# Kernel optimization log

Hardware: AMD Instinct MI355X
Metric: run time of the kernel (lower is better)

The kernel has to match this reference:

```python
import jax, jax.numpy as jnp
import numpy as np

B, S, H, NH, HD = 4, 4096, 1024, 16, 64

def setup_inputs() -> dict:
    key = jax.random.key(0)
    ks = jax.random.split(key, 5)
    scale = 1.0 / np.sqrt(H)
    return {
        "hidden_states": jax.random.normal(ks[0], (B, S, H), dtype=jnp.float32),
        "Wq": jax.random.normal(ks[1], (H, H), dtype=jnp.float32) * scale,
        "Wk": jax.random.normal(ks[2], (H, H), dtype=jnp.float32) * scale,
        "Wv": jax.random.normal(ks[3], (H, H), dtype=jnp.float32) * scale,
        "Wo": jax.random.normal(ks[4], (H, H), dtype=jnp.float32) * scale,
    }

def reference(hidden_states, Wq, Wk, Wv, Wo):
    b, s, h = hidden_states.shape
    # torch nn.Linear: y = x @ W.T
    q = (hidden_states @ Wq.T).reshape(b, s, NH, HD)
    k = (hidden_states @ Wk.T).reshape(b, s, NH, HD)
    v = (hidden_states @ Wv.T).reshape(b, s, NH, HD)
    # feature map: ELU (as in source, no +1)
    q = jax.nn.elu(q)
    k = jax.nn.elu(k)
    # per-head kv state: sum over sequence of outer products k_s v_s^T -> [b,h,d,e]
    kv = jnp.einsum('bshd,bshe->bhde', k, v)
    out = jnp.einsum('bqhd,bhde->bqhe', q, kv)  # [b,s,h,e]
    out = out.reshape(b, s, h)
    return out @ Wo.T  # dropout p=0.0 is identity
```

## Files before the change

kernel.cpp:

```cpp
#include <hip/hip_runtime.h>
#include <cstdint>
#include <cstddef>

#define B_  4
#define S_  4096
#define H_  1024
#define NH_ 16
#define M_  (B_*S_)

typedef __bf16 bf16x8 __attribute__((ext_vector_type(8)));
typedef float  f32x4  __attribute__((ext_vector_type(4)));

__device__ __forceinline__ unsigned short f2b(float f) {
  union { float f; unsigned u; } v; v.f = f;
  unsigned r = v.u + 0x7FFFu + ((v.u >> 16) & 1u);
  return (unsigned short)(r >> 16);
}
__device__ __forceinline__ float b2f(unsigned short u) {
  union { unsigned u; float f; } v; v.u = ((unsigned)u) << 16;
  return v.f;
}

#define GLD16(g, l) __builtin_amdgcn_global_load_lds( \
    (const __attribute__((address_space(1))) void*)(g), \
    (__attribute__((address_space(3))) void*)(l), 16, 0, 0)

#define VM0()  asm volatile("s_waitcnt vmcnt(0)" ::: "memory")
#define VM2()  asm volatile("s_waitcnt vmcnt(2)" ::: "memory")
#define VM4()  asm volatile("s_waitcnt vmcnt(4)" ::: "memory")
#define BAR()  do { asm volatile("" ::: "memory"); __builtin_amdgcn_s_barrier(); \
                    asm volatile("" ::: "memory"); } while (0)

__global__ void cast_f32_bf16(const float* __restrict__ src,
                              unsigned short* __restrict__ dst, int n4) {
  int i = blockIdx.x * blockDim.x + threadIdx.x;
  if (i >= n4) return;
  float4 f = reinterpret_cast<const float4*>(src)[i];
  ushort4 o;
  o.x = f2b(f.x); o.y = f2b(f.y); o.z = f2b(f.z); o.w = f2b(f.w);
  reinterpret_cast<ushort4*>(dst)[i] = o;
}

__global__ void cast_w4(const float* __restrict__ w0, const float* __restrict__ w1,
                        const float* __restrict__ w2, const float* __restrict__ w3,
                        unsigned short* __restrict__ dst) {
  int i = blockIdx.x * blockDim.x + threadIdx.x;
  int w = i >> 18, j = i & 0x3FFFF;
  const float* src = (w == 0) ? w0 : (w == 1) ? w1 : (w == 2) ? w2 : w3;
  float4 f = reinterpret_cast<const float4*>(src)[j];
  ushort4 o;
  o.x = f2b(f.x); o.y = f2b(f.y); o.z = f2b(f.z); o.w = f2b(f.w);
  reinterpret_cast<ushort4*>(dst)[i] = o;
}

template<int MODE>
__global__ __launch_bounds__(512, 2) void gemm256(
    const unsigned short* __restrict__ A_,
    const unsigned short* __restrict__ Bt_,
    void* __restrict__ out) {
  __shared__ __align__(16) unsigned short LDS[2][2][16384];

  const int NTN = (MODE == 0) ? 12 : 4;
  const int nx  = gridDim.x >> 3;
  const int b2  = (blockIdx.x & 7) * nx + (blockIdx.x >> 3);
  const int tileM = (b2 / NTN) << 8;
  const int tileN = (b2 % NTN) << 8;

  const unsigned short* Bt_e =
      (MODE == 1) ? (Bt_ + ((size_t)(tileM >> 12) << 20)) : Bt_;

  const int tid  = threadIdx.x;
  const int lane = tid & 63, wv = tid >> 6;
  const int wmi  = wv >> 2;
  const int wni  = wv & 3;
  const int fr   = lane & 15, fq = lane >> 4;

  const int sr0 = tid >> 3,          sc0 = (tid & 7) ^ (sr0 & 7);
  const int sr1 = (tid + 512) >> 3,  sc1 = (tid & 7) ^ (sr1 & 7);

#define STG(NB, ARR, HM, SRC, RB, TT) do {                                      \
    GLD16((SRC) + (size_t)((RB) + (HM)*128 + sr0) * 1024 + (TT)*64 + sc0*8,     \
          &LDS[NB][ARR][(HM)*8192 + wv*512]);                                   \
    GLD16((SRC) + (size_t)((RB) + (HM)*128 + sr1) * 1024 + (TT)*64 + sc1*8,     \
          &LDS[NB][ARR][(HM)*8192 + 4096 + wv*512]);                            \
  } while (0)

#define LOADA(CB, MQ) do {                                                      \
    _Pragma("unroll")                                                           \
    for (int m = 0; m < 4; m++) {                                               \
      int r = (MQ)*128 + wmi*64 + m*16 + fr;                                    \
      af[m][0] = *(const bf16x8*)&LDS[CB][0][r*64 + ((fq    ) ^ (r&7))*8];      \
      af[m][1] = *(const bf16x8*)&LDS[CB][0][r*64 + ((4 + fq) ^ (r&7))*8];      \
    }                                                                           \
  } while (0)

#define LOADB(CB, NQ) do {                                                      \
    _Pragma("unroll")                                                           \
    for (int n = 0; n < 2; n++) {                                               \
      int r = (NQ)*128 + wni*32 + n*16 + fr;                                    \
      bv[n][0] = *(const bf16x8*)&LDS[CB][1][r*64 + ((fq    ) ^ (r&7))*8];      \
      bv[n][1] = *(const bf16x8*)&LDS[CB][1][r*64 + ((4 + fq) ^ (r&7))*8];      \
    }                                                                           \
  } while (0)

#define MM(MQ, NQ) do {                                                         \
    __builtin_amdgcn_s_setprio(1);                                              \
    _Pragma("unroll")                                                           \
    for (int m = 0; m < 4; m++)                                                 \
      _Pragma("unroll")                                                         \
      for (int n = 0; n < 2; n++) {                                             \
        acc[MQ][NQ][m][n] = __builtin_amdgcn_mfma_f32_16x16x32_bf16(            \
            af[m][0], bv[n][0], acc[MQ][NQ][m][n], 0, 0, 0);                    \
        acc[MQ][NQ][m][n] = __builtin_amdgcn_mfma_f32_16x16x32_bf16(            \
            af[m][1], bv[n][1], acc[MQ][NQ][m][n], 0, 0, 0);                    \
      }                                                                         \
    __builtin_amdgcn_s_setprio(0);                                              \
  } while (0)

  f32x4 zero = {0.f, 0.f, 0.f, 0.f};
  f32x4 acc[2][2][4][2];
#pragma unroll
  for (int a = 0; a < 2; a++)
#pragma unroll
    for (int b = 0; b < 2; b++)
#pragma unroll
      for (int m = 0; m < 4; m++)
#pragma unroll
        for (int n = 0; n < 2; n++) acc[a][b][m][n] = zero;

  bf16x8 af[4][2], bv[2][2];

  STG(0, 0, 0, A_,   tileM, 0);
  STG(0, 0, 1, A_,   tileM, 0);
  STG(0, 1, 0, Bt_e, tileN, 0);
  STG(0, 1, 1, Bt_e, tileN, 0);
  VM0();
  BAR();

  int cb = 0;
  for (int t = 0; t < 15; ++t) {
    const int nb = cb ^ 1;
    LOADA(cb, 0); LOADB(cb, 0);
    STG(nb, 0, 0, A_,   tileM, t + 1);
    BAR(); MM(0, 0); VM4(); BAR();
    LOADB(cb, 1);
    STG(nb, 1, 0, Bt_e, tileN, t + 1);
    BAR(); MM(0, 1); VM4(); BAR();
    LOADA(cb, 1);
    STG(nb, 1, 1, Bt_e, tileN, t + 1);
    BAR(); MM(1, 1); BAR();
    LOADB(cb, 0);
    STG(nb, 0, 1, A_,   tileM, t + 1);
    BAR(); MM(1, 0); VM4(); BAR();
    cb = nb;
  }
  LOADA(cb, 0); LOADB(cb, 0);
  BAR(); MM(0, 0); VM2(); BAR();
  LOADB(cb, 1);
  BAR(); MM(0, 1); VM0(); BAR();
  LOADA(cb, 1);
  BAR(); MM(1, 1); BAR();
  LOADB(cb, 0);
  BAR(); MM(1, 0);

  if (MODE == 0) {
    unsigned short* Ep = &LDS[0][0][0];
    const int reg = tileN >> 10;
    const bool doELU = (reg < 2);
    BAR();
#pragma unroll
    for (int mq = 0; mq < 2; mq++)
#pragma unroll
      for (int nq = 0; nq < 2; nq++)
#pragma unroll
        for (int m = 0; m < 4; m++)
#pragma unroll
          for (int n = 0; n < 2; n++)
#pragma unroll
            for (int r = 0; r < 4; r++) {
              int row = mq * 128 + wmi * 64 + m * 16 + fq * 4 + r;
              int col = nq * 128 + wni * 32 + n * 16 + fr;
              float v = acc[mq][nq][m][n][r];
              if (doELU) v = v > 0.f ? v : (expf(v) - 1.f);
              Ep[row * 256 + (col ^ ((row & 7) << 3))] = f2b(v);
            }
    BAR();
    unsigned short* outp = (unsigned short*)out + (size_t)reg * M_ * H_;
    const int lcbase = tileN & 1023;
#pragma unroll
    for (int it = 0; it < 16; it++) {
      int g = it * 512 + tid;
      int row = g >> 5, col = (g & 31) * 8;
      bf16x8 val = *(const bf16x8*)&Ep[row * 256 + (col ^ ((row & 7) << 3))];
      *(bf16x8*)&outp[(size_t)(tileM + row) * H_ + lcbase + col] = val;
    }
  } else {
    float* Ef = (float*)&LDS[0][0][0];
#pragma unroll
    for (int mq = 0; mq < 2; mq++) {
      BAR();
#pragma unroll
      for (int nq = 0; nq < 2; nq++)
#pragma unroll
        for (int m = 0; m < 4; m++)
#pragma unroll
          for (int n = 0; n < 2; n++)
#pragma unroll
            for (int r = 0; r < 4; r++) {
              int row = wmi * 64 + m * 16 + fq * 4 + r;
              int col = nq * 128 + wni * 32 + n * 16 + fr;
              Ef[row * 256 + (col ^ ((row & 7) << 2))] = acc[mq][nq][m][n][r];
            }
      BAR();
#pragma unroll
      for (int it = 0; it < 16; it++) {
        int g = it * 512 + tid;
        int row = g >> 6, c = (g & 63) * 4;
        f32x4 val = *(const f32x4*)&Ef[row * 256 + (c ^ ((row & 7) << 2))];
        *(f32x4*)&((float*)out)[(size_t)(tileM + mq * 128 + row) * H_ + tileN + c] = val;
      }
    }
  }
#undef MM
#undef LOADB
#undef LOADA
#undef STG
}

__global__ __launch_bounds__(256) void kv_partial(
    const unsigned short* __restrict__ Kb,
    const unsigned short* __restrict__ Vb,
    float* __restrict__ kvp) {
  __shared__ __align__(16) unsigned short kt[32 * 64];
  __shared__ __align__(16) unsigned short vt[32 * 64];
  const int bh = blockIdx.x >> 3;
  const int ch = blockIdx.x & 7;
  const int b  = bh >> 4, h = bh & 15;
  const int t  = threadIdx.x;
  const int rr = t >> 3;
  const int cc = (t & 7) * 8;
  const int d0 = (t >> 4) * 4;
  const int e0 = (t & 15) * 4;

  float acc[4][4] = {};
  for (int s0 = ch * 512; s0 < ch * 512 + 512; s0 += 32) {
    size_t g = (size_t)(b * S_ + s0 + rr) * H_ + h * 64 + cc;
    *reinterpret_cast<uint4*>(&kt[rr * 64 + cc]) = *reinterpret_cast<const uint4*>(Kb + g);
    *reinterpret_cast<uint4*>(&vt[rr * 64 + cc]) = *reinterpret_cast<const uint4*>(Vb + g);
    __syncthreads();
#pragma unroll 4
    for (int ss = 0; ss < 32; ss++) {
      ushort4 k4 = *reinterpret_cast<const ushort4*>(&kt[ss * 64 + d0]);
      ushort4 v4 = *reinterpret_cast<const ushort4*>(&vt[ss * 64 + e0]);
      float kf[4] = {b2f(k4.x), b2f(k4.y), b2f(k4.z), b2f(k4.w)};
      float vf[4] = {b2f(v4.x), b2f(v4.y), b2f(v4.z), b2f(v4.w)};
#pragma unroll
      for (int i = 0; i < 4; i++)
#pragma unroll
        for (int j = 0; j < 4; j++) acc[i][j] += kf[i] * vf[j];
    }
    __syncthreads();
  }
  float* outp = kvp + (size_t)blockIdx.x * 4096;
#pragma unroll
  for (int i = 0; i < 4; i++)
#pragma unroll
    for (int j = 0; j < 4; j++) outp[(d0 + i) * 64 + e0 + j] = acc[i][j];
}

__global__ __launch_bounds__(256) void kv_reduce(
    const float* __restrict__ kvp, unsigned short* __restrict__ KVb) {
  const int bh = blockIdx.x;
#pragma unroll
  for (int i = 0; i < 16; i++) {
    int idx = threadIdx.x + i * 256;
    float s = 0.f;
#pragma unroll
    for (int ch = 0; ch < 8; ch++) s += kvp[(size_t)(bh * 8 + ch) * 4096 + idx];
    KVb[(size_t)bh * 4096 + idx] = f2b(s);
  }
}

__global__ __launch_bounds__(256) void merge_m(
    const unsigned short* __restrict__ KVb,
    const unsigned short* __restrict__ Wob,
    unsigned short* __restrict__ MbT) {
  const int bh = blockIdx.x >> 2;
  const int nc = blockIdx.x & 3;
  const int b  = bh >> 4, h = bh & 15;
  const int lane = threadIdx.x & 63, wv = threadIdx.x >> 6;
  const int fr = lane & 15, fq = lane >> 4;
  const int ncb = nc * 256 + wv * 64;

  f32x4 zero = {0.f, 0.f, 0.f, 0.f};
  f32x4 acc[4][4];
#pragma unroll
  for (int i = 0; i < 4; i++)
#pragma unroll
    for (int j = 0; j < 4; j++) acc[i][j] = zero;

#pragma unroll
  for (int kk = 0; kk < 2; kk++) {
    bf16x8 af[4], bvv[4];
#pragma unroll
    for (int i = 0; i < 4; i++)
      af[i] = *(const bf16x8*)&KVb[(size_t)bh * 4096 + (i * 16 + fr) * 64 + kk * 32 + fq * 8];
#pragma unroll
    for (int j = 0; j < 4; j++)
      bvv[j] = *(const bf16x8*)&Wob[(size_t)(ncb + j * 16 + fr) * 1024 + h * 64 + kk * 32 + fq * 8];
#pragma unroll
    for (int i = 0; i < 4; i++)
#pragma unroll
      for (int j = 0; j < 4; j++)
        acc[i][j] = __builtin_amdgcn_mfma_f32_16x16x32_bf16(af[i], bvv[j], acc[i][j], 0, 0, 0);
  }
#pragma unroll
  for (int i = 0; i < 4; i++)
#pragma unroll
    for (int j = 0; j < 4; j++)
#pragma unroll
      for (int r = 0; r < 4; r++) {
        int n = ncb + j * 16 + fr;
        int k = h * 64 + i * 16 + fq * 4 + r;
        MbT[((size_t)b << 20) + (size_t)n * 1024 + k] = f2b(acc[i][j][r]);
      }
}

extern "C" void kernel_launch(void* const* d_in, const int* in_sizes, int n_in,
                              void* d_out, int out_size, void* d_ws, size_t ws_size,
                              hipStream_t stream) {
  (void)in_sizes; (void)n_in; (void)out_size; (void)ws_size;
  const float* X  = (const float*)d_in[0];
  const float* Wq = (const float*)d_in[1];
  const float* Wk = (const float*)d_in[2];
  const float* Wv = (const float*)d_in[3];
  const float* Wo = (const float*)d_in[4];

  char*  ws  = (char*)d_ws;
  size_t off = 0;
  auto alloc = [&](size_t bytes) -> char* {
    char* p = ws + off;
    off += (bytes + 255) & ~(size_t)255;
    return p;
  };
  unsigned short* Xb   = (unsigned short*)alloc((size_t)M_ * H_ * 2);
  unsigned short* Wcat = (unsigned short*)alloc((size_t)4 * H_ * H_ * 2);
  unsigned short* QKVb = (unsigned short*)alloc((size_t)3 * M_ * H_ * 2);
  float*          kvp  = (float*)alloc((size_t)64 * 8 * 4096 * 4);
  unsigned short* KVb  = (unsigned short*)alloc((size_t)64 * 4096 * 2);
  unsigned short* MbT  = (unsigned short*)alloc((size_t)4 * H_ * H_ * 2);

  unsigned short* Qb = QKVb;
  unsigned short* Kb = QKVb + (size_t)M_ * H_;
  unsigned short* Vb = QKVb + (size_t)2 * M_ * H_;
  unsigned short* Wob = Wcat + (size_t)3 * H_ * H_;

  cast_f32_bf16<<<(M_ * H_) / 1024, 256, 0, stream>>>(X, Xb, (M_ * H_) / 4);
  cast_w4<<<(4 * H_ * H_) / 1024, 256, 0, stream>>>(Wq, Wk, Wv, Wo, Wcat);

  gemm256<0><<<768, 512, 0, stream>>>(Xb, Wcat, QKVb);

  kv_partial<<<512, 256, 0, stream>>>(Kb, Vb, kvp);
  kv_reduce<<<64, 256, 0, stream>>>(kvp, KVb);
  merge_m<<<256, 256, 0, stream>>>(KVb, Wob, MbT);

  gemm256<1><<<256, 512, 0, stream>>>(Qb, MbT, (float*)d_out);
}
```

Before: 259.6 us.

## Double-buffer GEMM fragment registers and prefetch next tile's LDS reads

Splits the A/B fragment registers into two sets so that LDS reads for the next quadrant, and for the next K-tile's first quadrant, are issued before the current MFMA block runs. This removes the barrier-bounded serial gaps between LDS reads and MFMAs. The change also reorders the initial global->LDS stages, relaxes vmcnt waits, and forces the main loop not to unroll. The extra fragment registers raise VGPR pressure, and the changed wait/barrier placement must still guard LDS buffer reuse correctly.

```diff
diff --git a/kernel.cpp b/kernel.cpp
--- a/kernel.cpp
+++ b/kernel.cpp
@@ -27,7 +27,6 @@
 
 #define VM0()  asm volatile("s_waitcnt vmcnt(0)" ::: "memory")
 #define VM2()  asm volatile("s_waitcnt vmcnt(2)" ::: "memory")
-#define VM4()  asm volatile("s_waitcnt vmcnt(4)" ::: "memory")
 #define BAR()  do { asm volatile("" ::: "memory"); __builtin_amdgcn_s_barrier(); \
                     asm volatile("" ::: "memory"); } while (0)
 
@@ -85,34 +84,34 @@
           &LDS[NB][ARR][(HM)*8192 + 4096 + wv*512]);                            \
   } while (0)
 
-#define LOADA(CB, MQ) do {                                                      \
+#define READA(CB, MQ, DST) do {                                                 \
     _Pragma("unroll")                                                           \
     for (int m = 0; m < 4; m++) {                                               \
       int r = (MQ)*128 + wmi*64 + m*16 + fr;                                    \
-      af[m][0] = *(const bf16x8*)&LDS[CB][0][r*64 + ((fq    ) ^ (r&7))*8];      \
-      af[m][1] = *(const bf16x8*)&LDS[CB][0][r*64 + ((4 + fq) ^ (r&7))*8];      \
+      DST[m][0] = *(const bf16x8*)&LDS[CB][0][r*64 + ((fq    ) ^ (r&7))*8];     \
+      DST[m][1] = *(const bf16x8*)&LDS[CB][0][r*64 + ((4 + fq) ^ (r&7))*8];     \
     }                                                                           \
   } while (0)
 
-#define LOADB(CB, NQ) do {                                                      \
+#define READB(CB, NQ, DST) do {                                                 \
     _Pragma("unroll")                                                           \
     for (int n = 0; n < 2; n++) {                                               \
       int r = (NQ)*128 + wni*32 + n*16 + fr;                                    \
-      bv[n][0] = *(const bf16x8*)&LDS[CB][1][r*64 + ((fq    ) ^ (r&7))*8];      \
-      bv[n][1] = *(const bf16x8*)&LDS[CB][1][r*64 + ((4 + fq) ^ (r&7))*8];      \
+      DST[n][0] = *(const bf16x8*)&LDS[CB][1][r*64 + ((fq    ) ^ (r&7))*8];     \
+      DST[n][1] = *(const bf16x8*)&LDS[CB][1][r*64 + ((4 + fq) ^ (r&7))*8];     \
     }                                                                           \
   } while (0)
 
-#define MM(MQ, NQ) do {                                                         \
+#define MMQ(MQ, NQ, AS, BS) do {                                                \
     __builtin_amdgcn_s_setprio(1);                                              \
     _Pragma("unroll")                                                           \
     for (int m = 0; m < 4; m++)                                                 \
       _Pragma("unroll")                                                         \
       for (int n = 0; n < 2; n++) {                                             \
         acc[MQ][NQ][m][n] = __builtin_amdgcn_mfma_f32_16x16x32_bf16(            \
-            af[m][0], bv[n][0], acc[MQ][NQ][m][n], 0, 0, 0);                    \
+            AS[m][0], BS[n][0], acc[MQ][NQ][m][n], 0, 0, 0);                    \
         acc[MQ][NQ][m][n] = __builtin_amdgcn_mfma_f32_16x16x32_bf16(            \
-            af[m][1], bv[n][1], acc[MQ][NQ][m][n], 0, 0, 0);                    \
+            AS[m][1], BS[n][1], acc[MQ][NQ][m][n], 0, 0, 0);                    \
       }                                                                         \
     __builtin_amdgcn_s_setprio(0);                                              \
   } while (0)
@@ -128,40 +127,45 @@
 #pragma unroll
         for (int n = 0; n < 2; n++) acc[a][b][m][n] = zero;
 
-  bf16x8 af[4][2], bv[2][2];
+  bf16x8 aA[4][2], aB[4][2], bA[2][2], bB[2][2];
 
   STG(0, 0, 0, A_,   tileM, 0);
-  STG(0, 0, 1, A_,   tileM, 0);
   STG(0, 1, 0, Bt_e, tileN, 0);
   STG(0, 1, 1, Bt_e, tileN, 0);
+  STG(0, 0, 1, A_,   tileM, 0);
   VM0();
   BAR();
+  READA(0, 0, aA); READB(0, 0, bA);
 
   int cb = 0;
+#pragma unroll 1
   for (int t = 0; t < 15; ++t) {
     const int nb = cb ^ 1;
-    LOADA(cb, 0); LOADB(cb, 0);
+    READB(cb, 1, bB);
     STG(nb, 0, 0, A_,   tileM, t + 1);
-    BAR(); MM(0, 0); VM4(); BAR();
-    LOADB(cb, 1);
+    VM2(); BAR();
+    MMQ(0, 0, aA, bA);
+    READA(cb, 1, aB);
     STG(nb, 1, 0, Bt_e, tileN, t + 1);
-    BAR(); MM(0, 1); VM4(); BAR();
-    LOADA(cb, 1);
+    BAR();
+    MMQ(0, 1, aA, bB);
     STG(nb, 1, 1, Bt_e, tileN, t + 1);
-    BAR(); MM(1, 1); BAR();
-    LOADB(cb, 0);
+    BAR();
+    MMQ(1, 1, aB, bB);
     STG(nb, 0, 1, A_,   tileM, t + 1);
-    BAR(); MM(1, 0); VM4(); BAR();
+    VM2(); BAR();
+    MMQ(1, 0, aB, bA);
+    READA(nb, 0, aA); READB(nb, 0, bA);
     cb = nb;
   }
-  LOADA(cb, 0); LOADB(cb, 0);
-  BAR(); MM(0, 0); VM2(); BAR();
-  LOADB(cb, 1);
-  BAR(); MM(0, 1); VM0(); BAR();
-  LOADA(cb, 1);
-  BAR(); MM(1, 1); BAR();
-  LOADB(cb, 0);
-  BAR(); MM(1, 0);
+  READB(cb, 1, bB); VM0(); BAR();
+  MMQ(0, 0, aA, bA);
+  READA(cb, 1, aB); BAR();
+  MMQ(0, 1, aA, bB);
+  BAR();
+  MMQ(1, 1, aB, bB);
+  BAR();
+  MMQ(1, 0, aB, bA);
 
   if (MODE == 0) {
     unsigned short* Ep = &LDS[0][0][0];
@@ -221,9 +225,9 @@
       }
     }
   }
-#undef MM
-#undef LOADB
-#undef LOADA
+#undef MMQ
+#undef READB
+#undef READA
 #undef STG
 }
 
```

Result: slower. 265.4 us (+2.2%).
